# Kernel tuning notes

Hardware: AMD Instinct MI355X
Metric: run time of the kernel (lower is better)

The kernel has to match this reference:

```python
import jax, jax.numpy as jnp
import numpy as np

B, S, H, D = 1, 4096, 16, 128
CAUSAL = True

def setup_inputs() -> dict:
    key = jax.random.key(0)
    kq, kk, kv = jax.random.split(key, 3)
    query = jax.random.normal(kq, (B, S, H, D), dtype=jnp.float32)
    k = jax.random.normal(kk, (B, S, H, D), dtype=jnp.float32)
    v = jax.random.normal(kv, (B, S, H, D), dtype=jnp.float32)
    return {"query": query, "key": k, "value": v}

def _attention(q, k, v):
    # q,k,v: [B, S, H, D] (flash-attn layout). Ulysses all2all + ring attention
    # compose to exact global attention; single-device reference is plain SDPA.
    scale = 1.0 / jnp.sqrt(jnp.asarray(q.shape[-1], q.dtype))
    scores = jnp.einsum("bshd,bthd->bhst", q, k) * scale  # [B,H,S,S]
    if CAUSAL:
        s = q.shape[1]
        mask = jnp.tril(jnp.ones((s, s), dtype=bool))
        scores = jnp.where(mask, scores, jnp.finfo(scores.dtype).min)
    probs = jax.nn.softmax(scores, axis=-1)
    return jnp.einsum("bhst,bthd->bshd", probs, v)

def reference(query, key, value):
    return _attention(query, key, value)
```

## Files before the change

### kernel.cpp

```cpp
#include <hip/hip_runtime.h>
#include <hip/hip_bf16.h>

typedef __bf16 bf16x8 __attribute__((ext_vector_type(8)));
typedef __bf16 bf16x4 __attribute__((ext_vector_type(4)));
typedef float  f32x4  __attribute__((ext_vector_type(4)));

#define SEQ   4096
#define NH    16
#define HD    128
#define KVB   32
#define NT32  128
#define STR   (NH * HD)
#define TE    4096
#define WSK   ((size_t)NH * NT32 * TE)
#define THRD  11.0f
#define MASKV -3.0e38f

__device__ __forceinline__ bf16x8 cvt_bf16x8(f32x4 a, f32x4 b, float s) {
    bf16x8 v;
    v[0] = (__bf16)(a[0]*s); v[1] = (__bf16)(a[1]*s);
    v[2] = (__bf16)(a[2]*s); v[3] = (__bf16)(a[3]*s);
    v[4] = (__bf16)(b[0]*s); v[5] = (__bf16)(b[1]*s);
    v[6] = (__bf16)(b[2]*s); v[7] = (__bf16)(b[7-7]*0.0f + b[3]*s);
    return v;
}

__global__ __launch_bounds__(256) void prep_kernel(
    const float* __restrict__ K, const float* __restrict__ V, __bf16* __restrict__ ws)
{
    const int tid = threadIdx.x;
    const int bid = blockIdx.x;
    const int h   = bid >> 7;
    const int t   = bid & 127;

    __bf16* kimg = ws + (size_t)(h*NT32 + t) * TE;
    __bf16* vimg = ws + WSK + (size_t)(h*NT32 + t) * TE;

    const int row = tid >> 3;
    #pragma unroll
    for (int u = 0; u < 2; ++u) {
        const int ch = (tid & 7)*2 + u;
        const float* src = K + (size_t)(t*KVB + row)*STR + h*HD + ch*8;
        f32x4 a = *(const f32x4*)src;
        f32x4 b = *(const f32x4*)(src + 4);
        const int e = (row*HD + ch*8) ^ ((row & 7) << 3);
        *(bf16x8*)&kimg[e] = cvt_bf16x8(a, b, 1.0f);
    }

    const int d4 = (tid & 31) * 4;
    const int pl = (tid >> 5) & 3;
    const int ih = tid >> 7;
    f32x4 va[4];
    #pragma unroll
    for (int r = 0; r < 4; ++r) {
        const int kr = t*KVB + 16*ih + 4*pl + r;
        va[r] = *(const f32x4*)(V + (size_t)kr*STR + h*HD + d4);
    }
    #pragma unroll
    for (int i4 = 0; i4 < 4; ++i4) {
        const int d = d4 + i4;
        bf16x4 w;
        w[0] = (__bf16)va[0][i4]; w[1] = (__bf16)va[1][i4];
        w[2] = (__bf16)va[2][i4]; w[3] = (__bf16)va[3][i4];
        const int e = d*KVB + 8*(pl ^ ((d >> 1) & 3)) + 4*ih;
        *(bf16x4*)&vimg[e] = w;
    }
}

__global__ __launch_bounds__(512) void fattn5_kernel(
    const float* __restrict__ Q, const __bf16* __restrict__ ws, float* __restrict__ O)
{
    __shared__ __align__(16) char ldsraw[66560];

    const int tid  = threadIdx.x;
    const int lane = tid & 63;
    const int wv   = tid >> 6;
    const int grp  = wv >> 2;
    const int wg   = wv & 3;
    const int c    = lane & 15;
    const int g    = lane >> 4;

    const int bid = blockIdx.x;
    const int h   = bid & 15;
    const int j   = bid >> 4;

    const __bf16* kws = ws;
    const __bf16* vws = ws + WSK;
    float* ml = (float*)(ldsraw + 65536);

    #define ISSUE(TT, BUF)  do {                                                       \
        const size_t tb_ = (size_t)(h*NT32 + (TT)) * TE;                               \
        _Pragma("unroll")                                                              \
        for (int ci = 0; ci < 4; ++ci) {                                               \
            const int fb = (4*wg + ci) * 1024;                                         \
            const __bf16* src = (fb < 8192) ? (kws + tb_ + (fb >> 1) + lane*8)         \
                                            : (vws + tb_ + ((fb - 8192) >> 1) + lane*8); \
            __builtin_amdgcn_global_load_lds(                                          \
                (const __attribute__((address_space(1))) void*)src,                    \
                (__attribute__((address_space(3))) void*)(ldsraw + grp*32768 + (BUF)*16384 + fb), \
                16, 0, 0);                                                             \
        }                                                                              \
    } while (0)

    const float scale = 0.08838834764831845f * 1.4426950408889634f;

    for (int ph = 0; ph < 2; ++ph) {
        const int qb  = ph ? j : (31 - j);
        const int q0  = qb * 128;
        const int qlo0 = q0 + 32*wg;
        const int nst = 2*qb + 2;
        const int tb0 = grp * nst;

        bf16x8 qf[2][4];
        #pragma unroll
        for (int sub = 0; sub < 2; ++sub) {
            const float* qrow = Q + (size_t)(qlo0 + 16*sub + c) * STR + h*HD;
            #pragma unroll
            for (int ks = 0; ks < 4; ++ks) {
                const int d0 = 32*ks + 8*g;
                qf[sub][ks] = cvt_bf16x8(*(const f32x4*)(qrow + d0), *(const f32x4*)(qrow + d0 + 4), scale);
            }
        }

        f32x4 oacc[2][8];
        #pragma unroll
        for (int s2 = 0; s2 < 2; ++s2)
            #pragma unroll
            for (int i = 0; i < 8; ++i) { oacc[s2][i][0]=0.f; oacc[s2][i][1]=0.f; oacc[s2][i][2]=0.f; oacc[s2][i][3]=0.f; }
        float mrow[2] = {-1e30f, -1e30f};
        float lrow[2] = {0.f, 0.f};

        int buf = 0;
        ISSUE(tb0, 0);

        for (int t = 0; t < nst; ++t) {
            __syncthreads();
            if (t + 1 < nst) ISSUE(tb0 + t + 1, buf ^ 1);

            const int k0 = (tb0 + t) * KVB;
            if (k0 <= qlo0 + 47) {
                const __bf16* bK = (const __bf16*)(ldsraw + grp*32768 + buf*16384);
                const __bf16* bV = bK + 4096;

                f32x4 s[2][2];
                #pragma unroll
                for (int a = 0; a < 2; ++a)
                    #pragma unroll
                    for (int b = 0; b < 2; ++b) { s[a][b][0]=0.f; s[a][b][1]=0.f; s[a][b][2]=0.f; s[a][b][3]=0.f; }
                __builtin_amdgcn_s_setprio(1);
                #pragma unroll
                for (int ks = 0; ks < 4; ++ks) {
                    const int e0 = (c*HD + 32*ks + 8*g) ^ ((c & 7) << 3);
                    bf16x8 ak0 = *(const bf16x8*)&bK[e0];
                    bf16x8 ak1 = *(const bf16x8*)&bK[e0 + 16*HD];
                    s[0][0] = __builtin_amdgcn_mfma_f32_16x16x32_bf16(ak0, qf[0][ks], s[0][0], 0, 0, 0);
                    s[0][1] = __builtin_amdgcn_mfma_f32_16x16x32_bf16(ak1, qf[0][ks], s[0][1], 0, 0, 0);
                    s[1][0] = __builtin_amdgcn_mfma_f32_16x16x32_bf16(ak0, qf[1][ks], s[1][0], 0, 0, 0);
                    s[1][1] = __builtin_amdgcn_mfma_f32_16x16x32_bf16(ak1, qf[1][ks], s[1][1], 0, 0, 0);
                }
                __builtin_amdgcn_s_setprio(0);

                if (k0 + 31 > qlo0) {
                    #pragma unroll
                    for (int sub = 0; sub < 2; ++sub) {
                        const int qg = qlo0 + 16*sub + c;
                        #pragma unroll
                        for (int r = 0; r < 4; ++r) {
                            if (k0 + 4*g + r > qg)      s[sub][0][r] = MASKV;
                            if (k0 + 16 + 4*g + r > qg) s[sub][1][r] = MASKV;
                        }
                    }
                }

                bf16x8 pa[2];
                #pragma unroll
                for (int sub = 0; sub < 2; ++sub) {
                    float pmax = fmaxf(fmaxf(fmaxf(s[sub][0][0],s[sub][0][1]), fmaxf(s[sub][0][2],s[sub][0][3])),
                                       fmaxf(fmaxf(s[sub][1][0],s[sub][1][1]), fmaxf(s[sub][1][2],s[sub][1][3])));
                    pmax = fmaxf(pmax, __shfl_xor(pmax, 16, 64));
                    pmax = fmaxf(pmax, __shfl_xor(pmax, 32, 64));
                    if (!__all(pmax - mrow[sub] <= THRD)) {
                        const float mn = fmaxf(mrow[sub], pmax);
                        const float alpha = exp2f(mrow[sub] - mn);
                        mrow[sub] = mn;
                        f32x4 aq;
                        #pragma unroll
                        for (int r = 0; r < 4; ++r) aq[r] = __shfl(alpha, 20*g + r, 64);
                        #pragma unroll
                        for (int dt = 0; dt < 8; ++dt) oacc[sub][dt] *= aq;
                        lrow[sub] *= alpha;
                    }
                    float rs = 0.f;
                    #pragma unroll
                    for (int r = 0; r < 4; ++r) {
                        s[sub][0][r] = exp2f(s[sub][0][r] - mrow[sub]); rs += s[sub][0][r];
                        s[sub][1][r] = exp2f(s[sub][1][r] - mrow[sub]); rs += s[sub][1][r];
                    }
                    rs += __shfl_xor(rs, 16, 64);
                    rs += __shfl_xor(rs, 32, 64);
                    lrow[sub] += rs;

                    pa[sub][0]=(__bf16)s[sub][0][0]; pa[sub][1]=(__bf16)s[sub][0][1];
                    pa[sub][2]=(__bf16)s[sub][0][2]; pa[sub][3]=(__bf16)s[sub][0][3];
                    pa[sub][4]=(__bf16)s[sub][1][0]; pa[sub][5]=(__bf16)s[sub][1][1];
                    pa[sub][6]=(__bf16)s[sub][1][2]; pa[sub][7]=(__bf16)s[sub][1][3];
                }

                __builtin_amdgcn_s_setprio(1);
                #pragma unroll
                for (int dt = 0; dt < 8; ++dt) {
                    const int d = 16*dt + c;
                    const int e = d*KVB + ((8*g) ^ (((d >> 1) & 3) << 3));
                    bf16x8 bv = *(const bf16x8*)&bV[e];
                    oacc[0][dt] = __builtin_amdgcn_mfma_f32_16x16x32_bf16(pa[0], bv, oacc[0][dt], 0, 0, 0);
                    oacc[1][dt] = __builtin_amdgcn_mfma_f32_16x16x32_bf16(pa[1], bv, oacc[1][dt], 0, 0, 0);
                }
                __builtin_amdgcn_s_setprio(0);
            }
            buf ^= 1;
        }

        __syncthreads();
        float* dump = (float*)ldsraw;
        if (grp == 1) {
            #pragma unroll
            for (int sub = 0; sub < 2; ++sub)
                if (lane < 16) {
                    ml[32*wg + 16*sub + c]       = mrow[sub];
                    ml[128 + 32*wg + 16*sub + c] = lrow[sub];
                }
            #pragma unroll
            for (int sub = 0; sub < 2; ++sub)
                #pragma unroll
                for (int dt = 0; dt < 8; ++dt)
                    #pragma unroll
                    for (int r = 0; r < 4; ++r)
                        dump[(32*wg + 16*sub + 4*g + r)*128 + 16*dt + c] = oacc[sub][dt][r];
        }
        __syncthreads();
        if (grp == 0) {
            #pragma unroll
            for (int sub = 0; sub < 2; ++sub) {
                const int ql = 32*wg + 16*sub;
                const float mB = ml[ql + c];
                const float lB = ml[128 + ql + c];
                const float mq = fmaxf(mrow[sub], mB);
                const float sA = exp2f(mrow[sub] - mq);
                const float sB = exp2f(mB - mq);
                const float inv = 1.0f / (lrow[sub]*sA + lB*sB);
                const float cA0 = sA * inv, cB0 = sB * inv;
                #pragma unroll
                for (int r = 0; r < 4; ++r) {
                    const float cA = __shfl(cA0, 20*g + r, 64);
                    const float cB = __shfl(cB0, 20*g + r, 64);
                    float* orow = O + (size_t)(q0 + ql + 4*g + r)*STR + h*HD;
                    #pragma unroll
                    for (int dt = 0; dt < 8; ++dt)
                        orow[16*dt + c] = oacc[sub][dt][r]*cA + dump[(ql + 4*g + r)*128 + 16*dt + c]*cB;
                }
            }
        }
        __syncthreads();
    }
    #undef ISSUE
}

extern "C" void kernel_launch(void* const* d_in, const int* in_sizes, int n_in,
                              void* d_out, int out_size, void* d_ws, size_t ws_size,
                              hipStream_t stream) {
    const float* Q = (const float*)d_in[0];
    const float* K = (const float*)d_in[1];
    const float* V = (const float*)d_in[2];
    float* O = (float*)d_out;

    prep_kernel<<<dim3(NH * NT32), dim3(256), 0, stream>>>(K, V, (__bf16*)d_ws);
    fattn5_kernel<<<dim3(16 * NH), dim3(512), 0, stream>>>(Q, (const __bf16*)d_ws, O);
}
```

Measured before the change: 145.5 us.

## Split each query block's KV range across four wave groups with tree merge

Doubles the workgroup to 1024 threads so four wave groups each process a quarter of the causal KV tiles, instead of two groups taking halves. Per-group partial outputs and max/sum statistics are combined through LDS in a two-level merge before the final normalized store. The goal is more waves per CU to hide latency and shorter per-wave KV loops. In exchange it raises LDS use to about 131 KB, adds extra barriers and merge traffic, and each block now needs the register budget of 1024 threads.

Result: slower. 304.1 us (+109.0%).

```diff
diff --git a/kernel.cpp b/kernel.cpp
--- a/kernel.cpp
+++ b/kernel.cpp
@@ -21,7 +21,7 @@
     v[0] = (__bf16)(a[0]*s); v[1] = (__bf16)(a[1]*s);
     v[2] = (__bf16)(a[2]*s); v[3] = (__bf16)(a[3]*s);
     v[4] = (__bf16)(b[0]*s); v[5] = (__bf16)(b[1]*s);
-    v[6] = (__bf16)(b[2]*s); v[7] = (__bf16)(b[7-7]*0.0f + b[3]*s);
+    v[6] = (__bf16)(b[2]*s); v[7] = (__bf16)(b[3]*s);
     return v;
 }
 
@@ -67,10 +67,10 @@
     }
 }
 
-__global__ __launch_bounds__(512) void fattn5_kernel(
+__global__ __launch_bounds__(1024) void fattn6_kernel(
     const float* __restrict__ Q, const __bf16* __restrict__ ws, float* __restrict__ O)
 {
-    __shared__ __align__(16) char ldsraw[66560];
+    __shared__ __align__(16) char ldsraw[134144];
 
     const int tid  = threadIdx.x;
     const int lane = tid & 63;
@@ -86,7 +86,7 @@
 
     const __bf16* kws = ws;
     const __bf16* vws = ws + WSK;
-    float* ml = (float*)(ldsraw + 65536);
+    float* ml = (float*)(ldsraw + 131072);
 
     #define ISSUE(TT, BUF)  do {                                                       \
         const size_t tb_ = (size_t)(h*NT32 + (TT)) * TE;                               \
@@ -105,11 +105,11 @@
     const float scale = 0.08838834764831845f * 1.4426950408889634f;
 
     for (int ph = 0; ph < 2; ++ph) {
-        const int qb  = ph ? j : (31 - j);
-        const int q0  = qb * 128;
+        const int qb   = ph ? j : (31 - j);
+        const int q0   = qb * 128;
         const int qlo0 = q0 + 32*wg;
-        const int nst = 2*qb + 2;
-        const int tb0 = grp * nst;
+        const int nst  = qb + 1;
+        const int tb0  = grp * nst;
 
         bf16x8 qf[2][4];
         #pragma unroll
@@ -130,8 +130,9 @@
         float mrow[2] = {-1e30f, -1e30f};
         float lrow[2] = {0.f, 0.f};
 
+        __syncthreads();
+        ISSUE(tb0, 0);
         int buf = 0;
-        ISSUE(tb0, 0);
 
         for (int t = 0; t < nst; ++t) {
             __syncthreads();
@@ -221,29 +222,70 @@
         }
 
         __syncthreads();
-        float* dump = (float*)ldsraw;
-        if (grp == 1) {
-            #pragma unroll
-            for (int sub = 0; sub < 2; ++sub)
+        float* dumpA = (float*)ldsraw;
+        float* dumpB = (float*)(ldsraw + 65536);
+
+        if (grp == 1 || grp == 3) {
+            float* dp = (grp == 1) ? dumpA : dumpB;
+            const int mo = (grp == 1) ? 0 : 2;
+            #pragma unroll
+            for (int sub = 0; sub < 2; ++sub) {
                 if (lane < 16) {
-                    ml[32*wg + 16*sub + c]       = mrow[sub];
-                    ml[128 + 32*wg + 16*sub + c] = lrow[sub];
-                }
-            #pragma unroll
-            for (int sub = 0; sub < 2; ++sub)
+                    ml[mo*128 + 32*wg + 16*sub + c]       = mrow[sub];
+                    ml[(mo+1)*128 + 32*wg + 16*sub + c]   = lrow[sub];
+                }
                 #pragma unroll
                 for (int dt = 0; dt < 8; ++dt)
                     #pragma unroll
                     for (int r = 0; r < 4; ++r)
-                        dump[(32*wg + 16*sub + 4*g + r)*128 + 16*dt + c] = oacc[sub][dt][r];
+                        dp[(32*wg + 16*sub + 4*g + r)*128 + 16*dt + c] = oacc[sub][dt][r];
+            }
+        }
+        __syncthreads();
+        if (grp == 0 || grp == 2) {
+            const float* dp = (grp == 0) ? dumpA : dumpB;
+            const int mo = (grp == 0) ? 0 : 2;
+            #pragma unroll
+            for (int sub = 0; sub < 2; ++sub) {
+                const float mB = ml[mo*128 + 32*wg + 16*sub + c];
+                const float lB = ml[(mo+1)*128 + 32*wg + 16*sub + c];
+                const float mq = fmaxf(mrow[sub], mB);
+                const float sA = exp2f(mrow[sub] - mq);
+                const float sB = exp2f(mB - mq);
+                lrow[sub] = lrow[sub]*sA + lB*sB;
+                mrow[sub] = mq;
+                #pragma unroll
+                for (int r = 0; r < 4; ++r) {
+                    const float sAr = __shfl(sA, 20*g + r, 64);
+                    const float sBr = __shfl(sB, 20*g + r, 64);
+                    #pragma unroll
+                    for (int dt = 0; dt < 8; ++dt)
+                        oacc[sub][dt][r] = oacc[sub][dt][r]*sAr
+                                         + dp[(32*wg + 16*sub + 4*g + r)*128 + 16*dt + c]*sBr;
+                }
+            }
+        }
+        __syncthreads();
+        if (grp == 2) {
+            #pragma unroll
+            for (int sub = 0; sub < 2; ++sub) {
+                if (lane < 16) {
+                    ml[4*128 + 32*wg + 16*sub + c] = mrow[sub];
+                    ml[5*128 + 32*wg + 16*sub + c] = lrow[sub];
+                }
+                #pragma unroll
+                for (int dt = 0; dt < 8; ++dt)
+                    #pragma unroll
+                    for (int r = 0; r < 4; ++r)
+                        dumpA[(32*wg + 16*sub + 4*g + r)*128 + 16*dt + c] = oacc[sub][dt][r];
+            }
         }
         __syncthreads();
         if (grp == 0) {
             #pragma unroll
             for (int sub = 0; sub < 2; ++sub) {
-                const int ql = 32*wg + 16*sub;
-                const float mB = ml[ql + c];
-                const float lB = ml[128 + ql + c];
+                const float mB = ml[4*128 + 32*wg + 16*sub + c];
+                const float lB = ml[5*128 + 32*wg + 16*sub + c];
                 const float mq = fmaxf(mrow[sub], mB);
                 const float sA = exp2f(mrow[sub] - mq);
                 const float sB = exp2f(mB - mq);
@@ -253,14 +295,14 @@
                 for (int r = 0; r < 4; ++r) {
                     const float cA = __shfl(cA0, 20*g + r, 64);
                     const float cB = __shfl(cB0, 20*g + r, 64);
-                    float* orow = O + (size_t)(q0 + ql + 4*g + r)*STR + h*HD;
+                    float* orow = O + (size_t)(q0 + 32*wg + 16*sub + 4*g + r)*STR + h*HD;
                     #pragma unroll
                     for (int dt = 0; dt < 8; ++dt)
-                        orow[16*dt + c] = oacc[sub][dt][r]*cA + dump[(ql + 4*g + r)*128 + 16*dt + c]*cB;
-                }
-            }
-        }
-        __syncthreads();
+                        orow[16*dt + c] = oacc[sub][dt][r]*cA
+                                        + dumpA[(32*wg + 16*sub + 4*g + r)*128 + 16*dt + c]*cB;
+                }
+            }
+        }
     }
     #undef ISSUE
 }
@@ -274,5 +316,5 @@
     float* O = (float*)d_out;
 
     prep_kernel<<<dim3(NH * NT32), dim3(256), 0, stream>>>(K, V, (__bf16*)d_ws);
-    fattn5_kernel<<<dim3(16 * NH), dim3(512), 0, stream>>>(Q, (const __bf16*)d_ws, O);
+    fattn6_kernel<<<dim3(16 * NH), dim3(1024), 0, stream>>>(Q, (const __bf16*)d_ws, O);
 }
```
